# Kernel tuning notes

Measured on AMD Instinct MI355X. Metric: run time of the kernel, lower is better.

The kernel has to match this reference:

```python
import jax, jax.numpy as jnp
import numpy as np

B, V, J, NB, NC = 4096, 778, 16, 10, 45
PARENTS = [0, 0, 1, 2, 0, 4, 5, 0, 7, 8, 0, 10, 11, 0, 13, 14]
TIPS = [745, 317, 444, 556, 673]
REORDER = [0, 13, 14, 15, 16, 1, 2, 3, 17, 4, 5, 6, 18, 10, 11, 12, 19, 7, 8, 9, 20]


def batch_rodrigues(axisang):
    # axisang: [N,3] -> rotation matrices [N,3,3] via quaternion, matching torch code
    angle = jnp.linalg.norm(axisang + 1e-8, axis=1, keepdims=True)
    axis = axisang / angle
    half = 0.5 * angle
    quat = jnp.concatenate([jnp.cos(half), jnp.sin(half) * axis], axis=1)
    quat = quat / jnp.linalg.norm(quat, axis=1, keepdims=True)
    w, x, y, z = quat[:, 0], quat[:, 1], quat[:, 2], quat[:, 3]
    w2, x2, y2, z2 = w * w, x * x, y * y, z * z
    wx, wy, wz = w * x, w * y, w * z
    xy, xz, yz = x * y, x * z, y * z
    rot = jnp.stack([
        w2 + x2 - y2 - z2, 2 * xy - 2 * wz, 2 * wy + 2 * xz,
        2 * wz + 2 * xy, w2 - x2 + y2 - z2, 2 * yz - 2 * wx,
        2 * xz - 2 * wy, 2 * wx + 2 * yz, w2 - x2 - y2 + z2], axis=1)
    return rot.reshape(-1, 3, 3)


def with_zeros(R, t):
    # R: [B,3,3], t: [B,3] -> homogeneous [B,4,4]
    top = jnp.concatenate([R, t[:, :, None]], axis=2)
    bottom = jnp.broadcast_to(jnp.array([0.0, 0.0, 0.0, 1.0], R.dtype), (R.shape[0], 1, 4))
    return jnp.concatenate([top, bottom], axis=1)


def setup_inputs() -> dict:
    key = jax.random.key(0)
    ks = jax.random.split(key, 10)
    th_J_regressor = jax.random.uniform(ks[6], (J, V), dtype=jnp.float32)
    th_J_regressor = th_J_regressor / th_J_regressor.sum(axis=1, keepdims=True)
    th_weights = jax.random.uniform(ks[7], (V, J), dtype=jnp.float32)
    th_weights = th_weights / th_weights.sum(axis=1, keepdims=True)
    return {
        'th_pose_coeffs': 0.3 * jax.random.normal(ks[0], (B, 3 + NC), dtype=jnp.float32),
        'th_betas': jax.random.normal(ks[1], (B, NB), dtype=jnp.float32),
        'th_trans': jax.random.normal(ks[2], (B, 3), dtype=jnp.float32),
        'th_shapedirs': 0.01 * jax.random.normal(ks[3], (V, 3, NB), dtype=jnp.float32),
        'th_posedirs': 0.01 * jax.random.normal(ks[4], (V, 3, 9 * (J - 1)), dtype=jnp.float32),
        'th_v_template': 0.1 * jax.random.normal(ks[5], (V, 3), dtype=jnp.float32),
        'th_J_regressor': th_J_regressor,
        'th_weights': th_weights,
        'th_selected_comps': jax.random.normal(ks[8], (NC, 45), dtype=jnp.float32),
        'th_hands_mean': jnp.zeros((45,), dtype=jnp.float32),  # flat_hand_mean=True
    }


def reference(th_pose_coeffs, th_betas, th_trans, th_shapedirs, th_posedirs,
              th_v_template, th_J_regressor, th_weights, th_selected_comps,
              th_hands_mean):
    b = th_pose_coeffs.shape[0]
    # PCA pose space -> full 45-dim axis-angle hand pose
    full_hand_pose = th_pose_coeffs[:, 3:3 + NC] @ th_selected_comps
    full_pose = jnp.concatenate(
        [th_pose_coeffs[:, :3], th_hands_mean[None] + full_hand_pose], axis=1)  # [B,48]
    rot_mats = batch_rodrigues(full_pose.reshape(-1, 3)).reshape(b, J, 3, 3)
    root_rot = rot_mats[:, 0]
    pose_map = (rot_mats[:, 1:] - jnp.eye(3, dtype=rot_mats.dtype)).reshape(b, 9 * (J - 1))
    v_shaped = jnp.einsum('vdk,bk->bvd', th_shapedirs, th_betas) + th_v_template[None]
    j = jnp.einsum('jv,bvd->bjd', th_J_regressor, v_shaped)  # [B,16,3]
    # pose blendshapes
    v_posed = v_shaped + jnp.einsum('vdp,bp->bvd', th_posedirs, pose_map)
    # kinematic chain (16 joints, fixed tree)
    transforms = [with_zeros(root_rot, j[:, 0])]
    for i in range(1, J):
        p = PARENTS[i]
        local = with_zeros(rot_mats[:, i], j[:, i] - j[:, p])
        transforms.append(jnp.matmul(transforms[p], local))
    results = jnp.stack(transforms, axis=1)  # [B,16,4,4]
    # remove rest-pose joint locations from translations
    j_h = jnp.concatenate([j, jnp.zeros((b, J, 1), j.dtype)], axis=2)
    corr = jnp.einsum('bjmn,bjn->bjm', results, j_h)  # [B,16,4]
    results2 = results - jnp.concatenate(
        [jnp.zeros(results.shape[:3] + (3,), results.dtype), corr[..., None]], axis=3)
    # linear blend skinning
    T = jnp.einsum('bjmn,vj->bvmn', results2, th_weights)  # [B,778,4,4]
    v_posed_h = jnp.concatenate([v_posed, jnp.ones((b, V, 1), v_posed.dtype)], axis=2)
    verts = jnp.einsum('bvmn,bvn->bvm', T, v_posed_h)[..., :3]  # [B,778,3]
    jtr = results[:, :, :3, 3]  # [B,16,3]
    jtr = jnp.concatenate([jtr, verts[:, TIPS]], axis=1)[:, REORDER]  # [B,21,3]
    verts = (verts + th_trans[:, None]) * 1000.0
    jtr = (jtr + th_trans[:, None]) * 1000.0
    return verts, jtr
```

## Files before the change

kernel.cpp:

```cpp
#include <hip/hip_runtime.h>
#include <hip/hip_bf16.h>
#include <cstddef>

#define B_      4096
#define V_      778
#define J_      16
#define NB_     10
#define NC_     45
#define NROWS   2334
#define PM_     135
#define KPW     192
#define NPW     2432
#define LDK     104

typedef __attribute__((ext_vector_type(8))) short short8v;
typedef __attribute__((ext_vector_type(4))) float f32x4;

#define WS_JS   0
#define WS_JT   480
#define WS_ROT  1024
#define WS_J    (WS_ROT + (size_t)B_*144)
#define WS_A2   (WS_J   + (size_t)B_*48)
#define WS_VP   (WS_A2  + (size_t)B_*192)
#define WS_ACT  (WS_VP  + (size_t)B_*NPW)
#define WS_BT   (WS_ACT + (size_t)B_*KPW/2)

__global__ __launch_bounds__(256) void k_js(const float* __restrict__ jreg,
                                            const float* __restrict__ shd,
                                            const float* __restrict__ tmpl,
                                            float* __restrict__ ws)
{
    int wid  = (blockIdx.x * 256 + threadIdx.x) >> 6;
    int lane = threadIdx.x & 63;
    if (wid >= 528) return;
    float s = 0.f;
    if (wid < 480) {
        int i = wid / 30, rem = wid % 30, d = rem / 10, k = rem % 10;
        const float* jr = jreg + i * V_;
        for (int v = lane; v < V_; v += 64) s += jr[v] * shd[v*30 + d*10 + k];
    } else {
        int e = wid - 480, i = e / 3, d = e % 3;
        const float* jr = jreg + i * V_;
        for (int v = lane; v < V_; v += 64) s += jr[v] * tmpl[v*3 + d];
    }
    #pragma unroll
    for (int off = 32; off; off >>= 1) s += __shfl_down(s, off, 64);
    if (lane == 0) ws[wid] = s;
}

__global__ __launch_bounds__(256) void k_bt(const float* __restrict__ shd,
                                            const float* __restrict__ pdr,
                                            __hip_bfloat16* __restrict__ BTg)
{
    int n = blockIdx.x;
    int k = threadIdx.x;
    if (k >= KPW) return;
    float v = 0.f;
    if (n < NROWS) {
        if (k < NB_)            v = shd[n * NB_ + k];
        else if (k < NB_ + PM_) v = pdr[(size_t)n * PM_ + (k - NB_)];
    }
    BTg[(size_t)n * KPW + k] = __float2bfloat16(v);
}

__global__ __launch_bounds__(256) void k_rod(const float* __restrict__ pc,
                                             const float* __restrict__ betas,
                                             const float* __restrict__ sc,
                                             const float* __restrict__ hm,
                                             float* __restrict__ ws,
                                             __hip_bfloat16* __restrict__ ACTg)
{
    __shared__ float scs[NC_*45 + 45];
    for (int i = threadIdx.x; i < NC_*45 + 45; i += 256)
        scs[i] = (i < NC_*45) ? sc[i] : hm[i - NC_*45];
    __syncthreads();

    int gid = blockIdx.x * 256 + threadIdx.x;
    int b = gid >> 4, i = gid & 15;
    const float* pcb = pc + b * 48;
    __hip_bfloat16* act = ACTg + (size_t)b * KPW;

    float a0, a1, a2;
    if (i == 0) { a0 = pcb[0]; a1 = pcb[1]; a2 = pcb[2]; }
    else {
        int col = (i - 1) * 3;
        float s0 = scs[NC_*45 + col], s1 = scs[NC_*45 + col + 1], s2 = scs[NC_*45 + col + 2];
        for (int k = 0; k < NC_; ++k) {
            float p = pcb[3 + k];
            s0 += p * scs[k*45 + col];
            s1 += p * scs[k*45 + col + 1];
            s2 += p * scs[k*45 + col + 2];
        }
        a0 = s0; a1 = s1; a2 = s2;
    }
    float e0 = a0 + 1e-8f, e1 = a1 + 1e-8f, e2 = a2 + 1e-8f;
    float angle = sqrtf(e0*e0 + e1*e1 + e2*e2);
    float inv  = 1.f / angle;
    float half = 0.5f * angle;
    float sh = sinf(half), ch = cosf(half);
    float w = ch, x = sh * a0 * inv, y = sh * a1 * inv, z = sh * a2 * inv;
    float qn = 1.f / sqrtf(w*w + x*x + y*y + z*z);
    w *= qn; x *= qn; y *= qn; z *= qn;
    float w2 = w*w, x2 = x*x, y2 = y*y, z2 = z*z;
    float wx = w*x, wy = w*y, wz = w*z, xy = x*y, xz = x*z, yz = y*z;
    float R[9] = { w2+x2-y2-z2, 2*xy-2*wz,   2*wy+2*xz,
                   2*wz+2*xy,   w2-x2+y2-z2, 2*yz-2*wx,
                   2*xz-2*wy,   2*wx+2*yz,   w2-x2-y2+z2 };

    float* rot = ws + WS_ROT + (size_t)b*144 + i*9;
    #pragma unroll
    for (int q = 0; q < 9; ++q) rot[q] = R[q];

    if (i == 0) {
        const float* bb = betas + b * NB_;
        #pragma unroll
        for (int k = 0; k < NB_; ++k) act[k] = __float2bfloat16(bb[k]);
        for (int k = NB_ + PM_; k < KPW; ++k) act[k] = __float2bfloat16(0.f);
    } else {
        #pragma unroll
        for (int q = 0; q < 9; ++q) {
            float pv = R[q] - ((q == 0 || q == 4 || q == 8) ? 1.f : 0.f);
            act[NB_ + (i-1)*9 + q] = __float2bfloat16(pv);
        }
    }
    const float* bb = betas + b * NB_;
    float* jout = ws + WS_J + (size_t)b*48 + i*3;
    #pragma unroll
    for (int d = 0; d < 3; ++d) {
        const float* jsrow = ws + WS_JS + (i*3 + d) * NB_;
        float s = ws[WS_JT + i*3 + d];
        #pragma unroll
        for (int k = 0; k < NB_; ++k) s += jsrow[k] * bb[k];
        jout[d] = s;
    }
}

__global__ __launch_bounds__(256) void k_chain(const float* __restrict__ trans,
                                               float* __restrict__ ws,
                                               float* __restrict__ out_jtr)
{
    int gid = blockIdx.x * 256 + threadIdx.x;
    int b = gid / 15, rem = gid % 15, f = rem / 3, m = rem % 3;
    const float* rot = ws + WS_ROT + (size_t)b*144;
    const float* j   = ws + WS_J   + (size_t)b*48;
    float* a2 = ws + WS_A2 + (size_t)b*192;
    float* jt = out_jtr + (size_t)b*63;
    const int INV[16] = {0,5,6,7,9,10,11,17,18,19,13,14,15,1,2,3};
    float trm = trans[b*3 + m];

    float j0x = j[0], j0y = j[1], j0z = j[2];
    float T0 = rot[m*3+0], T1 = rot[m*3+1], T2 = rot[m*3+2];
    float T3 = (m == 0) ? j0x : (m == 1) ? j0y : j0z;
    if (f == 0) {
        float corr = T0*j0x + T1*j0y + T2*j0z;
        a2[m*4+0] = T0; a2[m*4+1] = T1; a2[m*4+2] = T2; a2[m*4+3] = T3 - corr;
        jt[m] = (T3 + trm) * 1000.f;
    }
    float jpx = j0x, jpy = j0y, jpz = j0z;
    for (int s = 0; s < 3; ++s) {
        int i = f*3 + 1 + s;
        const float* R = rot + i*9;
        float jix = j[i*3], jiy = j[i*3+1], jiz = j[i*3+2];
        float d0 = jix - jpx, d1 = jiy - jpy, d2 = jiz - jpz;
        float n0 = T0*R[0] + T1*R[3] + T2*R[6];
        float n1 = T0*R[1] + T1*R[4] + T2*R[7];
        float n2 = T0*R[2] + T1*R[5] + T2*R[8];
        float n3 = T0*d0 + T1*d1 + T2*d2 + T3;
        T0 = n0; T1 = n1; T2 = n2; T3 = n3;
        float corr = T0*jix + T1*jiy + T2*jiz;
        a2[i*12 + m*4 + 0] = T0; a2[i*12 + m*4 + 1] = T1;
        a2[i*12 + m*4 + 2] = T2; a2[i*12 + m*4 + 3] = T3 - corr;
        jt[INV[i]*3 + m] = (T3 + trm) * 1000.f;
        jpx = jix; jpy = jiy; jpz = jiz;
    }
}

__global__ __launch_bounds__(256) void k_mfma(const __hip_bfloat16* __restrict__ ACTg,
                                              const __hip_bfloat16* __restrict__ BTg,
                                              const float* __restrict__ tmpl,
                                              float* __restrict__ vp)
{
    __shared__ ushort lA[128 * LDK];
    __shared__ ushort lB[128 * LDK];

    const int tid  = threadIdx.x;
    const int lane = tid & 63;
    const int wid  = tid >> 6;
    const int wm   = wid >> 1;
    const int wn   = wid & 1;
    const int b0   = blockIdx.y * 128;
    const int n0   = blockIdx.x * 128;
    const int l15  = lane & 15;
    const int lhi  = lane >> 4;

    f32x4 acc[4][4] = {};

    for (int kc = 0; kc < KPW; kc += 96) {
        #pragma unroll
        for (int it = 0; it < 6; ++it) {
            int idx = it * 256 + tid;
            int row = idx / 12, ch = idx % 12;
            const uint4* sa = (const uint4*)(ACTg + (size_t)(b0 + row) * KPW + kc + ch*8);
            *(uint4*)&lA[row*LDK + ch*8] = *sa;
            const uint4* sb = (const uint4*)(BTg + (size_t)(n0 + row) * KPW + kc + ch*8);
            *(uint4*)&lB[row*LDK + ch*8] = *sb;
        }
        __syncthreads();
        #pragma unroll
        for (int ks = 0; ks < 3; ++ks) {
            int kl = ks*32 + lhi*8;
            short8v a[4], bf[4];
            #pragma unroll
            for (int mt = 0; mt < 4; ++mt)
                a[mt] = *(const short8v*)&lA[(wm*64 + mt*16 + l15)*LDK + kl];
            #pragma unroll
            for (int nt = 0; nt < 4; ++nt)
                bf[nt] = *(const short8v*)&lB[(wn*64 + nt*16 + l15)*LDK + kl];
            #pragma unroll
            for (int mt = 0; mt < 4; ++mt)
                #pragma unroll
                for (int nt = 0; nt < 4; ++nt)
                    acc[mt][nt] = __builtin_amdgcn_mfma_f32_16x16x32_bf16(
                        a[mt], bf[nt], acc[mt][nt], 0, 0, 0);
        }
        __syncthreads();
    }
    #pragma unroll
    for (int nt = 0; nt < 4; ++nt) {
        int col = n0 + wn*64 + nt*16 + l15;
        float tv = (col < NROWS) ? tmpl[col] : 0.f;
        #pragma unroll
        for (int mt = 0; mt < 4; ++mt) {
            int rbase = b0 + wm*64 + mt*16 + lhi*4;
            #pragma unroll
            for (int r = 0; r < 4; ++r)
                vp[(size_t)(rbase + r) * NPW + col] = acc[mt][nt][r] + tv;
        }
    }
}

__global__ __launch_bounds__(256) void k_blend3(const float* __restrict__ wts,
                                                const float* __restrict__ trans,
                                                const float* __restrict__ ws,
                                                float* __restrict__ out)
{
    __shared__ float s_wt[16 * 64];
    __shared__ float s_a2[4 * 192];
    __shared__ float s_vp[4 * 192];
    const int tid = threadIdx.x;
    const int v0  = blockIdx.x * 64;
    const int b0  = blockIdx.y * 4;
    const int bl  = tid >> 6;
    const int vl  = tid & 63;
    const int b   = b0 + bl;
    const int v   = v0 + vl;

    {
        int vv = tid >> 2, q = tid & 3;
        int gv = v0 + vv;
        float4 wv = (gv < V_) ? *(const float4*)(wts + gv*16 + q*4)
                              : make_float4(0.f, 0.f, 0.f, 0.f);
        s_wt[(q*4+0)*64 + vv] = wv.x;
        s_wt[(q*4+1)*64 + vv] = wv.y;
        s_wt[(q*4+2)*64 + vv] = wv.z;
        s_wt[(q*4+3)*64 + vv] = wv.w;
    }
    if (tid < 192) {
        int bg = tid / 48, i = tid % 48;
        *(float4*)&s_a2[bg*192 + i*4] =
            *(const float4*)(ws + WS_A2 + (size_t)(b0 + bg)*192 + i*4);
        *(float4*)&s_vp[bg*192 + i*4] =
            *(const float4*)(ws + WS_VP + (size_t)(b0 + bg)*NPW + v0*3 + i*4);
    }
    __syncthreads();

    const float* a2r = &s_a2[bl * 192];
    float T[12] = {};
    #pragma unroll
    for (int jj = 0; jj < 16; ++jj) {
        float wj = s_wt[jj*64 + vl];
        float4 x0 = *(const float4*)&a2r[jj*12];
        float4 x1 = *(const float4*)&a2r[jj*12 + 4];
        float4 x2 = *(const float4*)&a2r[jj*12 + 8];
        T[0] += wj*x0.x; T[1] += wj*x0.y; T[2]  += wj*x0.z; T[3]  += wj*x0.w;
        T[4] += wj*x1.x; T[5] += wj*x1.y; T[6]  += wj*x1.z; T[7]  += wj*x1.w;
        T[8] += wj*x2.x; T[9] += wj*x2.y; T[10] += wj*x2.z; T[11] += wj*x2.w;
    }
    float p0 = s_vp[bl*192 + vl*3];
    float p1 = s_vp[bl*192 + vl*3 + 1];
    float p2 = s_vp[bl*192 + vl*3 + 2];
    float o0 = T[0]*p0 + T[1]*p1 + T[2]*p2  + T[3];
    float o1 = T[4]*p0 + T[5]*p1 + T[6]*p2  + T[7];
    float o2 = T[8]*p0 + T[9]*p1 + T[10]*p2 + T[11];

    float t0 = trans[b*3], t1 = trans[b*3+1], t2 = trans[b*3+2];
    float r0 = (o0 + t0)*1000.f, r1 = (o1 + t1)*1000.f, r2 = (o2 + t2)*1000.f;

    if (v < V_) {
        float* vo = out + (size_t)b*NROWS + v*3;
        vo[0] = r0; vo[1] = r1; vo[2] = r2;
        const int TIPS[5] = {745, 317, 444, 556, 673};
        const int TIPK[5] = {4, 8, 12, 16, 20};
        #pragma unroll
        for (int t = 0; t < 5; ++t) {
            if (v == TIPS[t]) {
                float* jt = out + (size_t)B_*NROWS + (size_t)b*63 + TIPK[t]*3;
                jt[0] = r0; jt[1] = r1; jt[2] = r2;
            }
        }
    }
}

extern "C" void kernel_launch(void* const* d_in, const int* in_sizes, int n_in,
                              void* d_out, int out_size, void* d_ws, size_t ws_size,
                              hipStream_t stream)
{
    const float* pc    = (const float*)d_in[0];
    const float* betas = (const float*)d_in[1];
    const float* trans = (const float*)d_in[2];
    const float* shd   = (const float*)d_in[3];
    const float* pdr   = (const float*)d_in[4];
    const float* tmpl  = (const float*)d_in[5];
    const float* jreg  = (const float*)d_in[6];
    const float* wts   = (const float*)d_in[7];
    const float* sc    = (const float*)d_in[8];
    const float* hm    = (const float*)d_in[9];
    float* out = (float*)d_out;
    float* ws  = (float*)d_ws;

    __hip_bfloat16* ACTg = (__hip_bfloat16*)(ws + WS_ACT);
    __hip_bfloat16* BTg  = (__hip_bfloat16*)(ws + WS_BT);
    float* vp = ws + WS_VP;

    hipLaunchKernelGGL(k_js,     dim3(132),       dim3(256), 0, stream, jreg, shd, tmpl, ws);
    hipLaunchKernelGGL(k_bt,     dim3(NPW),       dim3(256), 0, stream, shd, pdr, BTg);
    hipLaunchKernelGGL(k_rod,    dim3(B_*16/256), dim3(256), 0, stream, pc, betas, sc, hm, ws, ACTg);
    hipLaunchKernelGGL(k_chain,  dim3(B_*15/256), dim3(256), 0, stream, trans, ws,
                       out + (size_t)B_ * NROWS);
    hipLaunchKernelGGL(k_mfma,   dim3(19, 32),    dim3(256), 0, stream, ACTg, BTg, tmpl, vp);
    hipLaunchKernelGGL(k_blend3, dim3(13, B_/4),  dim3(256), 0, stream, wts, trans, ws, out);
}
```

Baseline: 150.2 us.

## Merge setup kernels and fuse Rodrigues with kinematic chain via shared memory

Combines the joint-regressor precompute and the bf16 weight-transpose kernels into one launch using block-index ranges. It also fuses the Rodrigues/joint kernel with the kinematic-chain kernel, keeping rotation matrices and joint positions in LDS instead of a global workspace round trip. This cuts two kernel launches and the global writes and reads of the rotation and joint buffers. The fused kernel uses more shared memory per block and leaves 16 threads idle in the chain phase.

New measurement: 144.4 us. -3.9%, faster.

```diff
diff --git a/kernel.cpp b/kernel.cpp
--- a/kernel.cpp
+++ b/kernel.cpp
@@ -18,19 +18,31 @@
 
 #define WS_JS   0
 #define WS_JT   480
-#define WS_ROT  1024
-#define WS_J    (WS_ROT + (size_t)B_*144)
-#define WS_A2   (WS_J   + (size_t)B_*48)
+#define WS_A2   1024
 #define WS_VP   (WS_A2  + (size_t)B_*192)
 #define WS_ACT  (WS_VP  + (size_t)B_*NPW)
-#define WS_BT   (WS_ACT + (size_t)B_*KPW/2)
-
-__global__ __launch_bounds__(256) void k_js(const float* __restrict__ jreg,
-                                            const float* __restrict__ shd,
-                                            const float* __restrict__ tmpl,
-                                            float* __restrict__ ws)
-{
-    int wid  = (blockIdx.x * 256 + threadIdx.x) >> 6;
+#define WS_BT   (WS_ACT + (size_t)B_*96)
+
+__global__ __launch_bounds__(256) void k_prep(const float* __restrict__ jreg,
+                                              const float* __restrict__ shd,
+                                              const float* __restrict__ pdr,
+                                              const float* __restrict__ tmpl,
+                                              float* __restrict__ ws,
+                                              __hip_bfloat16* __restrict__ BTg)
+{
+    int bx = blockIdx.x;
+    if (bx < NPW) {
+        int n = bx, k = threadIdx.x;
+        if (k >= KPW) return;
+        float v = 0.f;
+        if (n < NROWS) {
+            if (k < NB_)            v = shd[n * NB_ + k];
+            else if (k < NB_ + PM_) v = pdr[(size_t)n * PM_ + (k - NB_)];
+        }
+        BTg[(size_t)n * KPW + k] = __float2bfloat16(v);
+        return;
+    }
+    int wid  = ((bx - NPW) * 256 + threadIdx.x) >> 6;
     int lane = threadIdx.x & 63;
     if (wid >= 528) return;
     float s = 0.f;
@@ -48,101 +60,87 @@
     if (lane == 0) ws[wid] = s;
 }
 
-__global__ __launch_bounds__(256) void k_bt(const float* __restrict__ shd,
-                                            const float* __restrict__ pdr,
-                                            __hip_bfloat16* __restrict__ BTg)
-{
-    int n = blockIdx.x;
-    int k = threadIdx.x;
-    if (k >= KPW) return;
-    float v = 0.f;
-    if (n < NROWS) {
-        if (k < NB_)            v = shd[n * NB_ + k];
-        else if (k < NB_ + PM_) v = pdr[(size_t)n * PM_ + (k - NB_)];
-    }
-    BTg[(size_t)n * KPW + k] = __float2bfloat16(v);
-}
-
-__global__ __launch_bounds__(256) void k_rod(const float* __restrict__ pc,
-                                             const float* __restrict__ betas,
-                                             const float* __restrict__ sc,
-                                             const float* __restrict__ hm,
-                                             float* __restrict__ ws,
-                                             __hip_bfloat16* __restrict__ ACTg)
+__global__ __launch_bounds__(256) void k_pose(const float* __restrict__ pc,
+                                              const float* __restrict__ betas,
+                                              const float* __restrict__ sc,
+                                              const float* __restrict__ hm,
+                                              const float* __restrict__ trans,
+                                              float* __restrict__ ws,
+                                              __hip_bfloat16* __restrict__ ACTg,
+                                              float* __restrict__ out_jtr)
 {
     __shared__ float scs[NC_*45 + 45];
-    for (int i = threadIdx.x; i < NC_*45 + 45; i += 256)
+    __shared__ float sR[16 * 144];
+    __shared__ float sj[16 * 48];
+    const int tid = threadIdx.x;
+    for (int i = tid; i < NC_*45 + 45; i += 256)
         scs[i] = (i < NC_*45) ? sc[i] : hm[i - NC_*45];
     __syncthreads();
 
-    int gid = blockIdx.x * 256 + threadIdx.x;
-    int b = gid >> 4, i = gid & 15;
-    const float* pcb = pc + b * 48;
-    __hip_bfloat16* act = ACTg + (size_t)b * KPW;
-
-    float a0, a1, a2;
-    if (i == 0) { a0 = pcb[0]; a1 = pcb[1]; a2 = pcb[2]; }
-    else {
-        int col = (i - 1) * 3;
-        float s0 = scs[NC_*45 + col], s1 = scs[NC_*45 + col + 1], s2 = scs[NC_*45 + col + 2];
-        for (int k = 0; k < NC_; ++k) {
-            float p = pcb[3 + k];
-            s0 += p * scs[k*45 + col];
-            s1 += p * scs[k*45 + col + 1];
-            s2 += p * scs[k*45 + col + 2];
-        }
-        a0 = s0; a1 = s1; a2 = s2;
-    }
-    float e0 = a0 + 1e-8f, e1 = a1 + 1e-8f, e2 = a2 + 1e-8f;
-    float angle = sqrtf(e0*e0 + e1*e1 + e2*e2);
-    float inv  = 1.f / angle;
-    float half = 0.5f * angle;
-    float sh = sinf(half), ch = cosf(half);
-    float w = ch, x = sh * a0 * inv, y = sh * a1 * inv, z = sh * a2 * inv;
-    float qn = 1.f / sqrtf(w*w + x*x + y*y + z*z);
-    w *= qn; x *= qn; y *= qn; z *= qn;
-    float w2 = w*w, x2 = x*x, y2 = y*y, z2 = z*z;
-    float wx = w*x, wy = w*y, wz = w*z, xy = x*y, xz = x*z, yz = y*z;
-    float R[9] = { w2+x2-y2-z2, 2*xy-2*wz,   2*wy+2*xz,
-                   2*wz+2*xy,   w2-x2+y2-z2, 2*yz-2*wx,
-                   2*xz-2*wy,   2*wx+2*yz,   w2-x2-y2+z2 };
-
-    float* rot = ws + WS_ROT + (size_t)b*144 + i*9;
-    #pragma unroll
-    for (int q = 0; q < 9; ++q) rot[q] = R[q];
-
-    if (i == 0) {
+    {
+        int bl = tid >> 4, i = tid & 15;
+        int b  = blockIdx.x * 16 + bl;
+        const float* pcb = pc + b * 48;
+        __hip_bfloat16* act = ACTg + (size_t)b * KPW;
+
+        float a0, a1, a2;
+        if (i == 0) { a0 = pcb[0]; a1 = pcb[1]; a2 = pcb[2]; }
+        else {
+            int col = (i - 1) * 3;
+            float s0 = scs[NC_*45 + col], s1 = scs[NC_*45 + col + 1], s2 = scs[NC_*45 + col + 2];
+            for (int k = 0; k < NC_; ++k) {
+                float p = pcb[3 + k];
+                s0 += p * scs[k*45 + col];
+                s1 += p * scs[k*45 + col + 1];
+                s2 += p * scs[k*45 + col + 2];
+            }
+            a0 = s0; a1 = s1; a2 = s2;
+        }
+        float e0 = a0 + 1e-8f, e1 = a1 + 1e-8f, e2 = a2 + 1e-8f;
+        float angle = sqrtf(e0*e0 + e1*e1 + e2*e2);
+        float inv  = 1.f / angle;
+        float half = 0.5f * angle;
+        float sh = sinf(half), ch = cosf(half);
+        float w = ch, x = sh * a0 * inv, y = sh * a1 * inv, z = sh * a2 * inv;
+        float qn = 1.f / sqrtf(w*w + x*x + y*y + z*z);
+        w *= qn; x *= qn; y *= qn; z *= qn;
+        float w2 = w*w, x2 = x*x, y2 = y*y, z2 = z*z;
+        float wx = w*x, wy = w*y, wz = w*z, xy = x*y, xz = x*z, yz = y*z;
+        float R[9] = { w2+x2-y2-z2, 2*xy-2*wz,   2*wy+2*xz,
+                       2*wz+2*xy,   w2-x2+y2-z2, 2*yz-2*wx,
+                       2*xz-2*wy,   2*wx+2*yz,   w2-x2-y2+z2 };
+        #pragma unroll
+        for (int q = 0; q < 9; ++q) sR[bl*144 + i*9 + q] = R[q];
+
+        if (i == 0) {
+            const float* bb = betas + b * NB_;
+            #pragma unroll
+            for (int k = 0; k < NB_; ++k) act[k] = __float2bfloat16(bb[k]);
+            for (int k = NB_ + PM_; k < KPW; ++k) act[k] = __float2bfloat16(0.f);
+        } else {
+            #pragma unroll
+            for (int q = 0; q < 9; ++q) {
+                float pv = R[q] - ((q == 0 || q == 4 || q == 8) ? 1.f : 0.f);
+                act[NB_ + (i-1)*9 + q] = __float2bfloat16(pv);
+            }
+        }
         const float* bb = betas + b * NB_;
         #pragma unroll
-        for (int k = 0; k < NB_; ++k) act[k] = __float2bfloat16(bb[k]);
-        for (int k = NB_ + PM_; k < KPW; ++k) act[k] = __float2bfloat16(0.f);
-    } else {
-        #pragma unroll
-        for (int q = 0; q < 9; ++q) {
-            float pv = R[q] - ((q == 0 || q == 4 || q == 8) ? 1.f : 0.f);
-            act[NB_ + (i-1)*9 + q] = __float2bfloat16(pv);
-        }
-    }
-    const float* bb = betas + b * NB_;
-    float* jout = ws + WS_J + (size_t)b*48 + i*3;
-    #pragma unroll
-    for (int d = 0; d < 3; ++d) {
-        const float* jsrow = ws + WS_JS + (i*3 + d) * NB_;
-        float s = ws[WS_JT + i*3 + d];
-        #pragma unroll
-        for (int k = 0; k < NB_; ++k) s += jsrow[k] * bb[k];
-        jout[d] = s;
-    }
-}
-
-__global__ __launch_bounds__(256) void k_chain(const float* __restrict__ trans,
-                                               float* __restrict__ ws,
-                                               float* __restrict__ out_jtr)
-{
-    int gid = blockIdx.x * 256 + threadIdx.x;
-    int b = gid / 15, rem = gid % 15, f = rem / 3, m = rem % 3;
-    const float* rot = ws + WS_ROT + (size_t)b*144;
-    const float* j   = ws + WS_J   + (size_t)b*48;
+        for (int d = 0; d < 3; ++d) {
+            const float* jsrow = ws + WS_JS + (i*3 + d) * NB_;
+            float s = ws[WS_JT + i*3 + d];
+            #pragma unroll
+            for (int k = 0; k < NB_; ++k) s += jsrow[k] * bb[k];
+            sj[bl*48 + i*3 + d] = s;
+        }
+    }
+    __syncthreads();
+
+    if (tid >= 240) return;
+    int bl = tid / 15, rem = tid % 15, f = rem / 3, m = rem % 3;
+    int b  = blockIdx.x * 16 + bl;
+    const float* rot = &sR[bl * 144];
+    const float* j   = &sj[bl * 48];
     float* a2 = ws + WS_A2 + (size_t)b*192;
     float* jt = out_jtr + (size_t)b*63;
     const int INV[16] = {0,5,6,7,9,10,11,17,18,19,13,14,15,1,2,3};
@@ -332,10 +330,10 @@
     __hip_bfloat16* BTg  = (__hip_bfloat16*)(ws + WS_BT);
     float* vp = ws + WS_VP;
 
-    hipLaunchKernelGGL(k_js,     dim3(132),       dim3(256), 0, stream, jreg, shd, tmpl, ws);
-    hipLaunchKernelGGL(k_bt,     dim3(NPW),       dim3(256), 0, stream, shd, pdr, BTg);
-    hipLaunchKernelGGL(k_rod,    dim3(B_*16/256), dim3(256), 0, stream, pc, betas, sc, hm, ws, ACTg);
-    hipLaunchKernelGGL(k_chain,  dim3(B_*15/256), dim3(256), 0, stream, trans, ws,
+    hipLaunchKernelGGL(k_prep,   dim3(NPW + 132), dim3(256), 0, stream,
+                       jreg, shd, pdr, tmpl, ws, BTg);
+    hipLaunchKernelGGL(k_pose,   dim3(B_/16),     dim3(256), 0, stream,
+                       pc, betas, sc, hm, trans, ws, ACTg,
                        out + (size_t)B_ * NROWS);
     hipLaunchKernelGGL(k_mfma,   dim3(19, 32),    dim3(256), 0, stream, ACTg, BTg, tmpl, vp);
     hipLaunchKernelGGL(k_blend3, dim3(13, B_/4),  dim3(256), 0, stream, wts, trans, ws, out);
```
